# Performance work log

Measured on AMD Instinct MI355X. Metric: run time of the kernel, lower is better.

## Reference

```python
import jax, jax.numpy as jnp
import numpy as np


def setup_inputs() -> dict:
    key = jax.random.key(0)
    ks = jax.random.split(key, 6)
    B, T, U = 4, 160, 80
    De, Dd = 640, 640
    inner, vocab = 640, 1024
    return {
        "enc_state": jax.random.normal(ks[0], (B, T, De), jnp.float32),
        "dec_state": jax.random.normal(ks[1], (B, U, Dd), jnp.float32),
        "W1": jax.random.normal(ks[2], (De + Dd, inner), jnp.float32) * (1.0 / np.sqrt(De + Dd)),
        "b1": jax.random.normal(ks[3], (inner,), jnp.float32) * 0.02,
        "W2": jax.random.normal(ks[4], (inner, vocab), jnp.float32) * (1.0 / np.sqrt(inner)),
        "b2": jax.random.normal(ks[5], (vocab,), jnp.float32) * 0.02,
    }


def reference(enc_state, dec_state, W1, b1, W2, b2):
    # Faithful to: cat([enc tiled over U, dec tiled over T], -1) @ W1 + b1,
    # algebraically split so the [B,T,U,2D] concat is never materialized:
    # cat(e, d) @ W1 == e @ W1[:De] + d @ W1[De:]
    De = enc_state.shape[-1]
    W1_enc, W1_dec = W1[:De], W1[De:]
    enc_proj = jnp.einsum("btd,dh->bth", enc_state, W1_enc)   # [B,T,H]
    dec_proj = jnp.einsum("bud,dh->buh", dec_state, W1_dec)   # [B,U,H]
    # broadcast add over the (T,U) lattice -> [B,T,U,H]
    hidden = jnp.tanh(enc_proj[:, :, None, :] + dec_proj[:, None, :, :] + b1)
    logits = jnp.einsum("btuh,hv->btuv", hidden, W2) + b2     # [B,T,U,V]
    return logits
```

## Files before the change

### kernel.cpp

```cpp
#include <hip/hip_runtime.h>
#include <hip/hip_bf16.h>
#include <cstdint>

#define B_    4
#define T_    160
#define U_    80
#define D_    640
#define V_    1024
#define BT_   640
#define BU_   320
#define M_    51200

typedef __bf16 bf16x8 __attribute__((ext_vector_type(8)));
typedef float floatx4 __attribute__((ext_vector_type(4)));

__device__ __forceinline__ void g2l16(const void* g, void* l) {
    __builtin_amdgcn_global_load_lds((const __attribute__((address_space(1))) void*)g,
                                     (__attribute__((address_space(3))) void*)l,
                                     16, 0, 0);
}

__device__ __forceinline__ float fast_tanh(float x) {
    float e = __builtin_amdgcn_exp2f(x * 2.8853900817779268f);
    return 1.0f - 2.0f * __builtin_amdgcn_rcpf(e + 1.0f);
}

__global__ __launch_bounds__(256) void proj_kernel(
    const float* __restrict__ enc, const float* __restrict__ dec,
    const float* __restrict__ W1,
    float* __restrict__ encp, float* __restrict__ decp) {
    __shared__ float As[32][36];
    __shared__ float Ws[32][36];

    const int rt = blockIdx.y;
    const int ct = blockIdx.x;
    const float* Asrc;
    const float* Wsrc;
    float* Cdst;
    if (rt < 20) { Asrc = enc + (size_t)rt * 32 * D_;        Wsrc = W1;             Cdst = encp + (size_t)rt * 32 * D_; }
    else         { Asrc = dec + (size_t)(rt - 20) * 32 * D_; Wsrc = W1 + D_ * D_;   Cdst = decp + (size_t)(rt - 20) * 32 * D_; }

    const int tid = threadIdx.x;
    const int ar = tid >> 3, ac = (tid & 7) * 4;
    const int tr = tid >> 4, tc = tid & 15;

    float a00 = 0.f, a01 = 0.f, a10 = 0.f, a11 = 0.f;
    for (int k0 = 0; k0 < D_; k0 += 32) {
        __syncthreads();
        *(floatx4*)&As[ar][ac] = *(const floatx4*)&Asrc[(size_t)ar * D_ + k0 + ac];
        *(floatx4*)&Ws[ar][ac] = *(const floatx4*)&Wsrc[(size_t)(k0 + ar) * D_ + ct * 32 + ac];
        __syncthreads();
#pragma unroll
        for (int kk = 0; kk < 32; kk++) {
            float x0 = As[tr * 2][kk], x1 = As[tr * 2 + 1][kk];
            float w0 = Ws[kk][tc * 2], w1 = Ws[kk][tc * 2 + 1];
            a00 += x0 * w0; a01 += x0 * w1;
            a10 += x1 * w0; a11 += x1 * w1;
        }
    }
    const int cc = ct * 32 + tc * 2;
    Cdst[(size_t)(tr * 2) * D_ + cc]     = a00;
    Cdst[(size_t)(tr * 2) * D_ + cc + 1] = a01;
    Cdst[(size_t)(tr * 2 + 1) * D_ + cc]     = a10;
    Cdst[(size_t)(tr * 2 + 1) * D_ + cc + 1] = a11;
}

__global__ __launch_bounds__(256) void w2t_kernel(
    const float* __restrict__ W2, __bf16* __restrict__ W2t) {
    __shared__ __bf16 tile[32][33];
    const int vt = blockIdx.x;
    const int kt = blockIdx.y;
    const int tx = threadIdx.x & 31, ty = threadIdx.x >> 5;
#pragma unroll
    for (int i = 0; i < 4; i++)
        tile[ty + i * 8][tx] = (__bf16)W2[(size_t)(kt * 32 + ty + i * 8) * V_ + vt * 32 + tx];
    __syncthreads();
#pragma unroll
    for (int i = 0; i < 4; i++)
        W2t[(size_t)(vt * 32 + ty + i * 8) * D_ + kt * 32 + tx] = tile[tx][ty + i * 8];
}

__global__ __launch_bounds__(256) void hidden_kernel(
    const float* __restrict__ encp, const float* __restrict__ decp,
    const float* __restrict__ b1, __bf16* __restrict__ H) {
    const unsigned g = blockIdx.x * 256u + threadIdx.x;
    const unsigned row = g / 80u;
    const unsigned hg  = g % 80u;
    const unsigned u   = row % 80u;
    const unsigned bt  = row / 80u;
    const unsigned b   = bt / 160u;

    const float* ep = encp + (size_t)bt * D_ + hg * 8;
    const float* dp = decp + (size_t)(b * 80u + u) * D_ + hg * 8;
    const float* bp = b1 + hg * 8;

    floatx4 e0 = *(const floatx4*)ep,       e1 = *(const floatx4*)(ep + 4);
    floatx4 d0 = *(const floatx4*)dp,       d1 = *(const floatx4*)(dp + 4);
    floatx4 c0 = *(const floatx4*)bp,       c1 = *(const floatx4*)(bp + 4);

    bf16x8 hv;
#pragma unroll
    for (int i = 0; i < 4; i++) hv[i]     = (__bf16)fast_tanh(e0[i] + d0[i] + c0[i]);
#pragma unroll
    for (int i = 0; i < 4; i++) hv[i + 4] = (__bf16)fast_tanh(e1[i] + d1[i] + c1[i]);

    *(bf16x8*)(H + (size_t)g * 8) = hv;
}

__global__ __launch_bounds__(256) void gemm_kernel(
    const __bf16* __restrict__ H, const __bf16* __restrict__ W2t,
    const float* __restrict__ b2, float* __restrict__ C) {
    __shared__ __bf16 As[128 * 32];
    __shared__ __bf16 Bs[128 * 32];

    const int bx = blockIdx.x;
    const int nt = bx & 7;
    const int mt = bx >> 3;
    const int m0 = mt * 128, n0 = nt * 128;

    const int tid = threadIdx.x;
    const int lane = tid & 63;
    const int wave = tid >> 6;
    const int wm = (wave & 1) * 64, wn = (wave >> 1) * 64;
    const int lr = lane & 15, qd = lane >> 4;

    const int r = tid >> 2;
    const int c = (tid & 3) * 8;
    const __bf16* Ag = H   + (size_t)(m0 + r) * D_ + c;
    const __bf16* Bg = W2t + (size_t)(n0 + r) * D_ + c;
    __bf16* Al = &As[r * 32 + c];
    __bf16* Bl = &Bs[r * 32 + c];

    floatx4 acc[4][4] = {};

    for (int k0 = 0; k0 < D_; k0 += 32) {
        __syncthreads();
        g2l16(Ag + k0,                 Al);
        g2l16(Ag + k0 + 64 * D_,       Al + 64 * 32);
        g2l16(Bg + k0,                 Bl);
        g2l16(Bg + k0 + 64 * D_,       Bl + 64 * 32);
        __syncthreads();

        bf16x8 af[4], wf[4];
#pragma unroll
        for (int i = 0; i < 4; i++)
            af[i] = *(const bf16x8*)&As[(wm + i * 16 + lr) * 32 + qd * 8];
#pragma unroll
        for (int j = 0; j < 4; j++)
            wf[j] = *(const bf16x8*)&Bs[(wn + j * 16 + lr) * 32 + qd * 8];
#pragma unroll
        for (int i = 0; i < 4; i++)
#pragma unroll
            for (int j = 0; j < 4; j++)
                acc[i][j] = __builtin_amdgcn_mfma_f32_16x16x32_bf16(af[i], wf[j], acc[i][j], 0, 0, 0);
    }

    float bias[4];
#pragma unroll
    for (int j = 0; j < 4; j++) bias[j] = b2[n0 + wn + j * 16 + lr];
#pragma unroll
    for (int i = 0; i < 4; i++) {
#pragma unroll
        for (int j = 0; j < 4; j++) {
            const int col = n0 + wn + j * 16 + lr;
#pragma unroll
            for (int rg = 0; rg < 4; rg++) {
                const int row = m0 + wm + i * 16 + qd * 4 + rg;
                C[(size_t)row * V_ + col] = acc[i][j][rg] + bias[j];
            }
        }
    }
}

extern "C" void kernel_launch(void* const* d_in, const int* in_sizes, int n_in,
                              void* d_out, int out_size, void* d_ws, size_t ws_size,
                              hipStream_t stream) {
    const float* enc = (const float*)d_in[0];
    const float* dec = (const float*)d_in[1];
    const float* W1  = (const float*)d_in[2];
    const float* b1  = (const float*)d_in[3];
    const float* W2  = (const float*)d_in[4];
    const float* b2  = (const float*)d_in[5];
    float* out = (float*)d_out;

    char* ws = (char*)d_ws;
    float*  encp = (float*)ws;
    float*  decp = (float*)(ws + 1638400);
    __bf16* W2t  = (__bf16*)(ws + 1638400 + 819200);
    __bf16* Hbuf = (__bf16*)(ws + 1638400 + 819200 + 1310720);

    proj_kernel<<<dim3(20, 30), 256, 0, stream>>>(enc, dec, W1, encp, decp);
    w2t_kernel<<<dim3(32, 20), 256, 0, stream>>>(W2, W2t);
    hidden_kernel<<<16000, 256, 0, stream>>>(encp, decp, b1, Hbuf);
    gemm_kernel<<<3200, 256, 0, stream>>>(Hbuf, W2t, b2, out);
}
```

Baseline: 358.8 us.

## Rewrite W2 GEMM as 256x256 double-buffered, swizzled LDS pipeline with 8 waves

The main bf16 GEMM now uses 256x256 output tiles per 512-thread block. It double-buffers 64-wide K slices in 128 KB of LDS with an XOR swizzle against bank conflicts, and interleaves async global-to-LDS prefetch with MFMA phases. Manual vmcnt waits, barriers and setprio are used to keep the matrix units busy while loads are in flight. A block-index swizzle groups tiles for L2 reuse. The cost is heavy LDS use, which limits occupancy, plus more register pressure and a fragile hand-scheduled synchronisation scheme.

```diff
diff --git a/kernel.cpp b/kernel.cpp
--- a/kernel.cpp
+++ b/kernel.cpp
@@ -107,67 +107,103 @@
     *(bf16x8*)(H + (size_t)g * 8) = hv;
 }
 
-__global__ __launch_bounds__(256) void gemm_kernel(
+#define VM4  asm volatile("s_waitcnt vmcnt(4)" ::: "memory")
+#define VM0  asm volatile("s_waitcnt vmcnt(0)" ::: "memory")
+#define BAR  __builtin_amdgcn_s_barrier()
+#define SCB  __builtin_amdgcn_sched_barrier(0)
+
+#define STG_A(BUF, S, TL) do { \
+    g2l16(Hb + (unsigned)((S)*163840 + (TL)*128) + agl,         ldsp + (BUF)*32768 + (S)*16384 + stl); \
+    g2l16(Hb + (unsigned)((S)*163840 + (TL)*128 + 10240) + agl, ldsp + (BUF)*32768 + (S)*16384 + stl + 1024); \
+  } while (0)
+#define STG_B(BUF, S, TL) do { \
+    g2l16(Wb + (unsigned)((S)*163840 + (TL)*128) + agl,         ldsp + 65536 + (BUF)*32768 + (S)*16384 + stl); \
+    g2l16(Wb + (unsigned)((S)*163840 + (TL)*128 + 10240) + agl, ldsp + 65536 + (BUF)*32768 + (S)*16384 + stl + 1024); \
+  } while (0)
+
+#define PHASE(QM, QN, ABUF, BBUF, STAGE_STMT, WAIT_STMT) do { \
+    bf16x8 af0[4], af1[4], bg0[2], bg1[2]; \
+    _Pragma("unroll") for (int ii = 0; ii < 4; ++ii) { \
+      af0[ii] = *(const bf16x8*)(ldsp + (ABUF)*32768 + (QM)*16384 + ii*2048 + aRowB + sx0); \
+      af1[ii] = *(const bf16x8*)(ldsp + (ABUF)*32768 + (QM)*16384 + ii*2048 + aRowB + sx1); \
+    } \
+    _Pragma("unroll") for (int jj = 0; jj < 2; ++jj) { \
+      bg0[jj] = *(const bf16x8*)(ldsp + 65536 + (BBUF)*32768 + (QN)*16384 + jj*2048 + bRowB + sx0); \
+      bg1[jj] = *(const bf16x8*)(ldsp + 65536 + (BBUF)*32768 + (QN)*16384 + jj*2048 + bRowB + sx1); \
+    } \
+    STAGE_STMT; \
+    WAIT_STMT; \
+    BAR; SCB; \
+    __builtin_amdgcn_s_setprio(1); \
+    _Pragma("unroll") for (int ii = 0; ii < 4; ++ii) \
+      _Pragma("unroll") for (int jj = 0; jj < 2; ++jj) { \
+        acc[(QM)*4+ii][(QN)*2+jj] = __builtin_amdgcn_mfma_f32_16x16x32_bf16(af0[ii], bg0[jj], acc[(QM)*4+ii][(QN)*2+jj], 0, 0, 0); \
+        acc[(QM)*4+ii][(QN)*2+jj] = __builtin_amdgcn_mfma_f32_16x16x32_bf16(af1[ii], bg1[jj], acc[(QM)*4+ii][(QN)*2+jj], 0, 0, 0); \
+      } \
+    __builtin_amdgcn_s_setprio(0); \
+    BAR; SCB; \
+  } while (0)
+
+__global__ __launch_bounds__(512, 2) void gemm_kernel(
     const __bf16* __restrict__ H, const __bf16* __restrict__ W2t,
     const float* __restrict__ b2, float* __restrict__ C) {
-    __shared__ __bf16 As[128 * 32];
-    __shared__ __bf16 Bs[128 * 32];
-
-    const int bx = blockIdx.x;
-    const int nt = bx & 7;
-    const int mt = bx >> 3;
-    const int m0 = mt * 128, n0 = nt * 128;
+    __shared__ __align__(128) char lds[131072];
+
+    const int bid = blockIdx.x;
+    const int swz = (bid & 7) * 100 + (bid >> 3);
+    const int mt = swz >> 2, nt = swz & 3;
+    const int m0 = mt * 256, n0 = nt * 256;
 
     const int tid = threadIdx.x;
-    const int lane = tid & 63;
-    const int wave = tid >> 6;
-    const int wm = (wave & 1) * 64, wn = (wave >> 1) * 64;
-    const int lr = lane & 15, qd = lane >> 4;
-
-    const int r = tid >> 2;
-    const int c = (tid & 3) * 8;
-    const __bf16* Ag = H   + (size_t)(m0 + r) * D_ + c;
-    const __bf16* Bg = W2t + (size_t)(n0 + r) * D_ + c;
-    __bf16* Al = &As[r * 32 + c];
-    __bf16* Bl = &Bs[r * 32 + c];
-
-    floatx4 acc[4][4] = {};
-
-    for (int k0 = 0; k0 < D_; k0 += 32) {
-        __syncthreads();
-        g2l16(Ag + k0,                 Al);
-        g2l16(Ag + k0 + 64 * D_,       Al + 64 * 32);
-        g2l16(Bg + k0,                 Bl);
-        g2l16(Bg + k0 + 64 * D_,       Bl + 64 * 32);
-        __syncthreads();
-
-        bf16x8 af[4], wf[4];
-#pragma unroll
-        for (int i = 0; i < 4; i++)
-            af[i] = *(const bf16x8*)&As[(wm + i * 16 + lr) * 32 + qd * 8];
-#pragma unroll
-        for (int j = 0; j < 4; j++)
-            wf[j] = *(const bf16x8*)&Bs[(wn + j * 16 + lr) * 32 + qd * 8];
-#pragma unroll
-        for (int i = 0; i < 4; i++)
-#pragma unroll
-            for (int j = 0; j < 4; j++)
-                acc[i][j] = __builtin_amdgcn_mfma_f32_16x16x32_bf16(af[i], wf[j], acc[i][j], 0, 0, 0);
+    const int w = tid >> 6, l = tid & 63;
+    const int wr = w >> 2, wc = w & 3;
+    const int lrow = l & 15, lk = l >> 4, l7 = l & 7, lhi = l >> 3;
+
+    const unsigned swzb = (unsigned)(((l & 7) ^ lhi) * 16);
+    const unsigned agl  = (unsigned)((w * 16 + lhi) * 1280) + swzb;
+    const unsigned stl  = (unsigned)(w * 2048 + l * 16);
+
+    const char* Hb = (const char*)H   + (size_t)m0 * 1280;
+    const char* Wb = (const char*)W2t + (size_t)n0 * 1280;
+    char* ldsp = (char*)lds;
+
+    const unsigned aRowB = (unsigned)((wr * 64 + lrow) * 128);
+    const unsigned bRowB = (unsigned)(wc * 4096 + lrow * 128);
+    const unsigned sx0 = (unsigned)(((0 + lk) ^ l7) * 16);
+    const unsigned sx1 = (unsigned)(((4 + lk) ^ l7) * 16);
+
+    floatx4 acc[8][4] = {};
+
+    STG_A(0, 0, 0); STG_A(0, 1, 0); STG_B(0, 0, 0); STG_B(0, 1, 0);
+    STG_A(1, 0, 1); STG_B(1, 0, 1);
+    VM4; BAR; SCB;
+
+#pragma unroll 1
+    for (int it = 0; it < 5; ++it) {
+        const int t1 = 2 * it + 1, t2 = 2 * it + 2, t3 = 2 * it + 3;
+        const bool pf = (it < 4);
+        PHASE(0, 0, 0, 0, { STG_A(1, 1, t1); STG_B(1, 1, t1); }, (void)0);
+        PHASE(0, 1, 0, 0, (void)0, (void)0);
+        PHASE(1, 0, 0, 0, { if (pf) STG_A(0, 0, t2); }, (void)0);
+        PHASE(1, 1, 0, 0, { if (pf) STG_B(0, 0, t2); },
+                          { if (it == 4) { VM0; } else { VM4; } });
+        PHASE(0, 0, 1, 1, { if (pf) { STG_A(0, 1, t2); STG_B(0, 1, t2); } }, (void)0);
+        PHASE(0, 1, 1, 1, (void)0, (void)0);
+        PHASE(1, 0, 1, 1, { if (pf) STG_A(1, 0, t3); }, (void)0);
+        PHASE(1, 1, 1, 1, { if (pf) STG_B(1, 0, t3); }, VM4);
     }
 
-    float bias[4];
-#pragma unroll
-    for (int j = 0; j < 4; j++) bias[j] = b2[n0 + wn + j * 16 + lr];
-#pragma unroll
-    for (int i = 0; i < 4; i++) {
-#pragma unroll
-        for (int j = 0; j < 4; j++) {
-            const int col = n0 + wn + j * 16 + lr;
-#pragma unroll
-            for (int rg = 0; rg < 4; rg++) {
-                const int row = m0 + wm + i * 16 + qd * 4 + rg;
-                C[(size_t)row * V_ + col] = acc[i][j][rg] + bias[j];
-            }
+#pragma unroll
+    for (int j = 0; j < 4; ++j) {
+        const int col = n0 + (j >> 1) * 128 + wc * 32 + (j & 1) * 16 + lrow;
+        const float bj = b2[col];
+#pragma unroll
+        for (int i = 0; i < 8; ++i) {
+            const int row = m0 + (i >> 2) * 128 + wr * 64 + (i & 3) * 16 + lk * 4;
+            float* Cp = C + (size_t)row * V_ + col;
+#pragma unroll
+            for (int rg = 0; rg < 4; ++rg)
+                Cp[(size_t)rg * V_] = acc[i][j][rg] + bj;
         }
     }
 }
@@ -192,5 +228,5 @@
     proj_kernel<<<dim3(20, 30), 256, 0, stream>>>(enc, dec, W1, encp, decp);
     w2t_kernel<<<dim3(32, 20), 256, 0, stream>>>(W2, W2t);
     hidden_kernel<<<16000, 256, 0, stream>>>(encp, decp, b1, Hbuf);
-    gemm_kernel<<<3200, 256, 0, stream>>>(Hbuf, W2t, b2, out);
-}
+    gemm_kernel<<<800, 512, 0, stream>>>(Hbuf, W2t, b2, out);
+}
```

New measurement: 345.3 us. -3.8%, faster.
